# Optimization experiments

Measured on AMD Instinct MI355X. Metric: run time of the kernel, lower is better.

The kernel has to match this reference:

```python
import jax, jax.numpy as jnp
import numpy as np


def setup_inputs() -> dict:
    key = jax.random.key(0)
    ks = jax.random.split(key, 9)
    B, S, E, H, D = 8, 1000, 1024, 16, 64
    sc = 0.02
    return {
        "x": jax.random.normal(ks[0], (B, S, E), dtype=jnp.float32),
        "wq": jax.random.normal(ks[1], (H, E, D), dtype=jnp.float32) * sc,
        "bq": jax.random.normal(ks[2], (H, D), dtype=jnp.float32) * sc,
        "wk": jax.random.normal(ks[3], (H, E, D), dtype=jnp.float32) * sc,
        "bk": jax.random.normal(ks[4], (H, D), dtype=jnp.float32) * sc,
        "wv": jax.random.normal(ks[5], (H, E, D), dtype=jnp.float32) * sc,
        "bv": jax.random.normal(ks[6], (H, D), dtype=jnp.float32) * sc,
        "wp": jax.random.normal(ks[7], (E, E), dtype=jnp.float32) * sc,
        "bp": jax.random.normal(ks[8], (E,), dtype=jnp.float32) * sc,
    }


def reference(x, wq, bq, wk, bk, wv, bv, wp, bp):
    B, S, E = x.shape
    H, _, D = wq.shape
    # per-head projections, all heads batched: [B,H,S,D]
    q = jnp.einsum('bse,hed->bhsd', x, wq) + bq[None, :, None, :]
    k = jnp.einsum('bse,hed->bhsd', x, wk) + bk[None, :, None, :]
    v = jnp.einsum('bse,hed->bhsd', x, wv) + bv[None, :, None, :]
    # NOTE: original scales by sqrt(seq_len), not sqrt(head_dim)
    scores = jnp.einsum('bhsd,bhtd->bhst', q, k) / jnp.asarray(S, x.dtype) ** 0.5
    causal = jnp.tril(jnp.ones((S, S), dtype=bool))  # mask[:S,:S] == 1 keeps
    scores = jnp.where(causal, scores, jnp.asarray(-jnp.inf, x.dtype))
    attn = jax.nn.softmax(scores, axis=-1)
    z = jnp.einsum('bhst,bhtd->bhsd', attn, v)
    # concat heads in head order -> [B,S,E]
    y = z.transpose(0, 2, 1, 3).reshape(B, S, E)
    # projection then exact GELU (dropout is identity at eval)
    return jax.nn.gelu(jnp.einsum('bse,ef->bsf', y, wp) + bp, approximate=False)
```

## Files before the change

### kernel.cpp

```cpp
#include <hip/hip_runtime.h>
#include <hip/hip_bf16.h>
#include <math.h>

constexpr int B_ = 8, S_ = 1000, E_ = 1024, H_ = 16, D_ = 64;
constexpr int M_ = B_ * S_;

using bf16x8 = __attribute__((ext_vector_type(8))) __bf16;
using u16x8  = __attribute__((ext_vector_type(8))) unsigned short;
using f32x4  = __attribute__((ext_vector_type(4))) float;

static __device__ __forceinline__ unsigned short f2bf(float f) {
    union { float f; unsigned u; } c; c.f = f;
    return (unsigned short)((c.u + 0x7FFF + ((c.u >> 16) & 1)) >> 16);
}
static __device__ __forceinline__ unsigned short f2bf_fast(float f) {
    union { float f; unsigned u; } c; c.f = f;
    return (unsigned short)((c.u + 0x8000) >> 16);
}
static __device__ __forceinline__ float bfr2f(unsigned short s) {
    union { unsigned u; float f; } c; c.u = ((unsigned)s) << 16;
    return c.f;
}

__global__ __launch_bounds__(256) void cast_x_kernel(
    const float* __restrict__ x, unsigned short* __restrict__ xbf)
{
    const size_t i = ((size_t)blockIdx.x * 256 + threadIdx.x) * 4;
    float4 v = *(const float4*)(x + i);
    ushort4 o;
    o.x = f2bf(v.x); o.y = f2bf(v.y); o.z = f2bf(v.z); o.w = f2bf(v.w);
    *(ushort4*)(xbf + i) = o;
}

__global__ __launch_bounds__(256) void transpose_wqkv_kernel(
    const float* __restrict__ wq, const float* __restrict__ wk,
    const float* __restrict__ wv, unsigned short* __restrict__ WT)
{
    __shared__ unsigned short Ts[64 * 65];
    const int et = blockIdx.x, zh = blockIdx.y;
    const int z = zh >> 4, h = zh & 15;
    const float* src = (z == 0 ? wq : z == 1 ? wk : wv) + (size_t)h * E_ * D_;

    const int d = threadIdx.x & 63;
    const int e0 = threadIdx.x >> 6;
    #pragma unroll
    for (int p = 0; p < 16; ++p) {
        const int e = e0 + p * 4;
        Ts[d * 65 + e] = f2bf(src[(size_t)(et * 64 + e) * D_ + d]);
    }
    __syncthreads();
    const int e = threadIdx.x & 63;
    const int d0 = threadIdx.x >> 6;
    #pragma unroll
    for (int p = 0; p < 16; ++p) {
        const int dd = d0 + p * 4;
        WT[((size_t)zh * 64 + dd) * E_ + et * 64 + e] = Ts[dd * 65 + e];
    }
}

__global__ __launch_bounds__(256) void transpose_wp_kernel(
    const float* __restrict__ wp, unsigned short* __restrict__ wpT)
{
    __shared__ unsigned short Ts[64 * 65];
    const int et = blockIdx.x, ft = blockIdx.y;
    const int f = threadIdx.x & 63;
    const int e0 = threadIdx.x >> 6;
    #pragma unroll
    for (int p = 0; p < 16; ++p) {
        const int e = e0 + p * 4;
        Ts[f * 65 + e] = f2bf(wp[(size_t)(et * 64 + e) * E_ + ft * 64 + f]);
    }
    __syncthreads();
    const int e = threadIdx.x & 63;
    const int f0 = threadIdx.x >> 6;
    #pragma unroll
    for (int p = 0; p < 16; ++p) {
        const int ff = f0 + p * 4;
        wpT[((size_t)(ft * 64 + ff)) * E_ + et * 64 + e] = Ts[ff * 65 + e];
    }
}

__global__ __launch_bounds__(256) void transpose_v_kernel(
    const unsigned short* __restrict__ vb, unsigned short* __restrict__ vt)
{
    __shared__ unsigned short Ts[64 * 65];
    const int st = blockIdx.x, bh = blockIdx.y;
    const size_t ibase = (size_t)bh * S_ * D_;
    const size_t obase = (size_t)bh * D_ * S_;

    const int d = threadIdx.x & 63;
    const int s0 = threadIdx.x >> 6;
    #pragma unroll
    for (int p = 0; p < 16; ++p) {
        const int s = s0 + p * 4;
        const int srow = st * 64 + s;
        Ts[s * 65 + d] = (srow < S_) ? vb[ibase + (size_t)srow * D_ + d] : 0;
    }
    __syncthreads();
    const int s = threadIdx.x & 63;
    const int d0 = threadIdx.x >> 6;
    const int scol = st * 64 + s;
    if (scol < S_) {
        #pragma unroll
        for (int p = 0; p < 16; ++p) {
            const int dd = d0 + p * 4;
            vt[obase + (size_t)dd * S_ + scol] = Ts[s * 65 + dd];
        }
    }
}

__global__ __launch_bounds__(256) void qkv_mfma_kernel(
    const unsigned short* __restrict__ xbf, const unsigned short* __restrict__ WT,
    const float* __restrict__ bq, const float* __restrict__ bk,
    const float* __restrict__ bv,
    unsigned short* __restrict__ qb, unsigned short* __restrict__ kb,
    unsigned short* __restrict__ vb)
{
    constexpr int P = 72;
    __shared__ unsigned short As[128 * P];
    __shared__ unsigned short Bs[3][64 * P];

    const int tid = threadIdx.x;
    const int wave = tid >> 6, lane = tid & 63;
    const int m16 = lane & 15, quad = lane >> 4;
    const int m0 = blockIdx.x * 128;
    const int h  = blockIdx.y;

    f32x4 acc[3][4][2];
    #pragma unroll
    for (int z = 0; z < 3; ++z)
        #pragma unroll
        for (int nt = 0; nt < 4; ++nt)
            #pragma unroll
            for (int mh = 0; mh < 2; ++mh)
                acc[z][nt][mh] = (f32x4){0.f, 0.f, 0.f, 0.f};

    const int ar = tid & 31;
    const int ac8 = (tid >> 5) * 8;
    const int bd = tid & 63;
    const int bc8 = (tid >> 6) * 8;

    for (int kk = 0; kk < E_; kk += 64) {
        __syncthreads();
        #pragma unroll
        for (int p = 0; p < 4; ++p) {
            const int r = ar + p * 32;
            int srow = m0 + r; if (srow >= M_) srow = M_ - 1;
            *(u16x8*)&As[r * P + ac8] =
                *(const u16x8*)(xbf + (size_t)srow * E_ + kk + ac8);
        }
        #pragma unroll
        for (int z = 0; z < 3; ++z) {
            const unsigned short* wb = WT + ((size_t)(z * 16 + h) * 64 + bd) * E_ + kk;
            *(u16x8*)&Bs[z][bd * P + bc8]      = *(const u16x8*)(wb + bc8);
            *(u16x8*)&Bs[z][bd * P + bc8 + 32] = *(const u16x8*)(wb + bc8 + 32);
        }
        __syncthreads();

        #pragma unroll
        for (int kh = 0; kh < 2; ++kh) {
            const int ko = kh * 32 + quad * 8;
            const bf16x8 a0 = *(const bf16x8*)&As[(wave * 32 + m16) * P + ko];
            const bf16x8 a1 = *(const bf16x8*)&As[(wave * 32 + 16 + m16) * P + ko];
            #pragma unroll
            for (int z = 0; z < 3; ++z)
                #pragma unroll
                for (int nt = 0; nt < 4; ++nt) {
                    const bf16x8 bfr = *(const bf16x8*)&Bs[z][(nt * 16 + m16) * P + ko];
                    acc[z][nt][0] = __builtin_amdgcn_mfma_f32_16x16x32_bf16(a0, bfr, acc[z][nt][0], 0, 0, 0);
                    acc[z][nt][1] = __builtin_amdgcn_mfma_f32_16x16x32_bf16(a1, bfr, acc[z][nt][1], 0, 0, 0);
                }
        }
    }

    float biasv[3][4];
    #pragma unroll
    for (int nt = 0; nt < 4; ++nt) {
        biasv[0][nt] = bq[h * D_ + nt * 16 + m16];
        biasv[1][nt] = bk[h * D_ + nt * 16 + m16];
        biasv[2][nt] = bv[h * D_ + nt * 16 + m16];
    }

    #pragma unroll
    for (int mh = 0; mh < 2; ++mh)
        #pragma unroll
        for (int r = 0; r < 4; ++r) {
            const int row = m0 + wave * 32 + mh * 16 + quad * 4 + r;
            if (row < M_) {
                const int b = row / S_, s = row % S_;
                const size_t ob = (((size_t)b * H_ + h) * S_ + s) * D_ + m16;
                #pragma unroll
                for (int nt = 0; nt < 4; ++nt) {
                    qb[ob + nt * 16] = f2bf(acc[0][nt][mh][r] + biasv[0][nt]);
                    kb[ob + nt * 16] = f2bf(acc[1][nt][mh][r] + biasv[1][nt]);
                    vb[ob + nt * 16] = f2bf(acc[2][nt][mh][r] + biasv[2][nt]);
                }
            }
        }
}

__global__ __launch_bounds__(256) void attn_flash_kernel(
    const unsigned short* __restrict__ q, const unsigned short* __restrict__ k,
    const unsigned short* __restrict__ vt, unsigned short* __restrict__ ybf)
{
    constexpr int P_ = 72;
    __shared__ unsigned short Qs[64 * P_];
    __shared__ unsigned short Ks[64 * P_];
    __shared__ unsigned short Vt[64 * P_];
    __shared__ unsigned short Ps[4][16 * P_];

    const int tid  = threadIdx.x;
    const int wave = tid >> 6, lane = tid & 63;
    const int m16  = lane & 15, quad = lane >> 4;
    const int qt = (int)gridDim.x - 1 - (int)blockIdx.x;
    const int h = blockIdx.y, b = blockIdx.z;
    const size_t bh  = ((size_t)b * H_ + h) * S_;
    const size_t vtb = ((size_t)b * H_ + h) * (size_t)D_ * S_;
    const float sl2e = 0.031622776601683794f * 1.4426950408889634f;

    const int c8 = (tid & 7) * 8;
    const int r0 = tid >> 3;

    #pragma unroll
    for (int rr = 0; rr < 64; rr += 32) {
        const int r = r0 + rr;
        const int srow = qt * 64 + r;
        u16x8 val = {0, 0, 0, 0, 0, 0, 0, 0};
        if (srow < S_) val = *(const u16x8*)(q + (bh + srow) * D_ + c8);
        u16x8 o;
        #pragma unroll
        for (int j = 0; j < 8; ++j) o[j] = f2bf_fast(bfr2f(val[j]) * sl2e);
        *(u16x8*)&Qs[r * P_ + c8] = o;
    }
    __syncthreads();

    const bf16x8 qa0 = *(const bf16x8*)&Qs[(wave * 16 + m16) * P_ + quad * 8];
    const bf16x8 qa1 = *(const bf16x8*)&Qs[(wave * 16 + m16) * P_ + 32 + quad * 8];

    f32x4 O[4] = {{0,0,0,0},{0,0,0,0},{0,0,0,0},{0,0,0,0}};
    float l_i[4] = {0.f, 0.f, 0.f, 0.f};

    const int qrow_base = qt * 64 + wave * 16 + quad * 4;

    u16x8 kreg[2], vreg[2];
    #pragma unroll
    for (int i = 0; i < 2; ++i) {
        const int srow = r0 + i * 32;
        kreg[i] = *(const u16x8*)(k + (bh + srow) * D_ + c8);
        vreg[i] = *(const u16x8*)(vt + vtb + (size_t)(r0 + i * 32) * S_ + c8);
    }

    for (int tt = 0; tt <= qt; ++tt) {
        const int t0 = tt * 64;
        __syncthreads();
        #pragma unroll
        for (int i = 0; i < 2; ++i) {
            *(u16x8*)&Ks[(r0 + i * 32) * P_ + c8] = kreg[i];
            *(u16x8*)&Vt[(r0 + i * 32) * P_ + c8] = vreg[i];
        }
        __syncthreads();

        if (tt < qt) {
            const int nt0 = t0 + 64;
            #pragma unroll
            for (int i = 0; i < 2; ++i) {
                const int t = r0 + i * 32;
                const int srow = nt0 + t;
                u16x8 kv = {0,0,0,0,0,0,0,0}, vv = {0,0,0,0,0,0,0,0};
                if (srow < S_) kv = *(const u16x8*)(k + (bh + srow) * D_ + c8);
                if (nt0 + c8 < S_)
                    vv = *(const u16x8*)(vt + vtb + (size_t)t * S_ + nt0 + c8);
                kreg[i] = kv; vreg[i] = vv;
            }
        }

        f32x4 sc[4];
        #pragma unroll
        for (int ts = 0; ts < 4; ++ts) {
            const bf16x8 kb0 = *(const bf16x8*)&Ks[(ts * 16 + m16) * P_ + quad * 8];
            const bf16x8 kb1 = *(const bf16x8*)&Ks[(ts * 16 + m16) * P_ + 32 + quad * 8];
            f32x4 a = {0.f, 0.f, 0.f, 0.f};
            a = __builtin_amdgcn_mfma_f32_16x16x32_bf16(qa0, kb0, a, 0, 0, 0);
            a = __builtin_amdgcn_mfma_f32_16x16x32_bf16(qa1, kb1, a, 0, 0, 0);
            sc[ts] = a;
        }

        unsigned short* const pw = &Ps[wave][0];
        if (tt == qt) {
            #pragma unroll
            for (int ts = 0; ts < 4; ++ts) {
                const int t = t0 + ts * 16 + m16;
                #pragma unroll
                for (int r = 0; r < 4; ++r) {
                    float p = __builtin_amdgcn_exp2f(sc[ts][r]);
                    p = (t <= qrow_base + r) ? p : 0.f;
                    pw[(quad * 4 + r) * P_ + ts * 16 + m16] = f2bf_fast(p);
                    l_i[r] += p;
                }
            }
        } else {
            #pragma unroll
            for (int ts = 0; ts < 4; ++ts)
                #pragma unroll
                for (int r = 0; r < 4; ++r) {
                    const float p = __builtin_amdgcn_exp2f(sc[ts][r]);
                    pw[(quad * 4 + r) * P_ + ts * 16 + m16] = f2bf_fast(p);
                    l_i[r] += p;
                }
        }

        const bf16x8 pa0 = *(const bf16x8*)&pw[m16 * P_ + quad * 8];
        const bf16x8 pa1 = *(const bf16x8*)&pw[m16 * P_ + 32 + quad * 8];
        #pragma unroll
        for (int db = 0; db < 4; ++db) {
            const bf16x8 vb0 = *(const bf16x8*)&Vt[(db * 16 + m16) * P_ + quad * 8];
            const bf16x8 vb1 = *(const bf16x8*)&Vt[(db * 16 + m16) * P_ + 32 + quad * 8];
            O[db] = __builtin_amdgcn_mfma_f32_16x16x32_bf16(pa0, vb0, O[db], 0, 0, 0);
            O[db] = __builtin_amdgcn_mfma_f32_16x16x32_bf16(pa1, vb1, O[db], 0, 0, 0);
        }
    }

    #pragma unroll
    for (int off = 1; off < 16; off <<= 1)
        #pragma unroll
        for (int r = 0; r < 4; ++r)
            l_i[r] += __shfl_xor(l_i[r], off, 64);

    #pragma unroll
    for (int r = 0; r < 4; ++r) {
        const int qrow = qrow_base + r;
        if (qrow < S_) {
            const float invl = 1.0f / l_i[r];
            #pragma unroll
            for (int db = 0; db < 4; ++db)
                ybf[((size_t)b * S_ + qrow) * E_ + h * D_ + db * 16 + m16] =
                    f2bf(O[db][r] * invl);
        }
    }
}

__global__ __launch_bounds__(256) void proj_mfma_kernel(
    const unsigned short* __restrict__ ybf, const unsigned short* __restrict__ wpT,
    const float* __restrict__ bp, float* __restrict__ out)
{
    constexpr int P = 72;
    __shared__ unsigned short As[128 * P];
    __shared__ unsigned short Bs[128 * P];

    const int tid = threadIdx.x;
    const int wave = tid >> 6, lane = tid & 63;
    const int m16 = lane & 15, quad = lane >> 4;
    const int wm = wave >> 1, wn = wave & 1;
    const int m0 = blockIdx.x * 128;
    const int n0 = blockIdx.y * 128;

    f32x4 acc[4][4];
    #pragma unroll
    for (int nf = 0; nf < 4; ++nf)
        #pragma unroll
        for (int mf = 0; mf < 4; ++mf)
            acc[nf][mf] = (f32x4){0.f, 0.f, 0.f, 0.f};

    const int ar = tid & 31;
    const int ac8 = (tid >> 5) * 8;

    int asrow[4];
    #pragma unroll
    for (int p = 0; p < 4; ++p) {
        int r = m0 + ar + p * 32;
        asrow[p] = (r < M_) ? r : (M_ - 1);
    }

    u16x8 areg[4], breg[4];
    #pragma unroll
    for (int p = 0; p < 4; ++p) {
        areg[p] = *(const u16x8*)(ybf + (size_t)asrow[p] * E_ + ac8);
        breg[p] = *(const u16x8*)(wpT + (size_t)(n0 + ar + p * 32) * E_ + ac8);
    }

    for (int kk = 0; kk < E_; kk += 64) {
        __syncthreads();
        #pragma unroll
        for (int p = 0; p < 4; ++p) {
            *(u16x8*)&As[(ar + p * 32) * P + ac8] = areg[p];
            *(u16x8*)&Bs[(ar + p * 32) * P + ac8] = breg[p];
        }
        __syncthreads();

        if (kk + 64 < E_) {
            const int kn = kk + 64;
            #pragma unroll
            for (int p = 0; p < 4; ++p) {
                areg[p] = *(const u16x8*)(ybf + (size_t)asrow[p] * E_ + kn + ac8);
                breg[p] = *(const u16x8*)(wpT + (size_t)(n0 + ar + p * 32) * E_ + kn + ac8);
            }
        }

        #pragma unroll
        for (int kh = 0; kh < 2; ++kh) {
            const int ko = kh * 32 + quad * 8;
            bf16x8 af[4];
            #pragma unroll
            for (int mf = 0; mf < 4; ++mf)
                af[mf] = *(const bf16x8*)&As[(wm * 64 + mf * 16 + m16) * P + ko];
            #pragma unroll
            for (int nf = 0; nf < 4; ++nf) {
                const bf16x8 bfr = *(const bf16x8*)&Bs[(wn * 64 + nf * 16 + m16) * P + ko];
                #pragma unroll
                for (int mf = 0; mf < 4; ++mf)
                    acc[nf][mf] = __builtin_amdgcn_mfma_f32_16x16x32_bf16(
                        af[mf], bfr, acc[nf][mf], 0, 0, 0);
            }
        }
    }

    float biasv[4];
    #pragma unroll
    for (int nf = 0; nf < 4; ++nf)
        biasv[nf] = bp[n0 + wn * 64 + nf * 16 + m16];

    #pragma unroll
    for (int mf = 0; mf < 4; ++mf)
        #pragma unroll
        for (int r = 0; r < 4; ++r) {
            const int row = m0 + wm * 64 + mf * 16 + quad * 4 + r;
            if (row < M_) {
                #pragma unroll
                for (int nf = 0; nf < 4; ++nf) {
                    const int col = n0 + wn * 64 + nf * 16 + m16;
                    const float t = acc[nf][mf][r] + biasv[nf];
                    const float g = 0.5f * t * (1.0f + erff(t * 0.70710678118654752f));
                    out[(size_t)row * E_ + col] = g;
                }
            }
        }
}

extern "C" void kernel_launch(void* const* d_in, const int* in_sizes, int n_in,
                              void* d_out, int out_size, void* d_ws, size_t ws_size,
                              hipStream_t stream)
{
    const float* x  = (const float*)d_in[0];
    const float* wq = (const float*)d_in[1];
    const float* bq = (const float*)d_in[2];
    const float* wk = (const float*)d_in[3];
    const float* bk = (const float*)d_in[4];
    const float* wv = (const float*)d_in[5];
    const float* bv = (const float*)d_in[6];
    const float* wp = (const float*)d_in[7];
    const float* bp = (const float*)d_in[8];
    float* out = (float*)d_out;

    const size_t nME = (size_t)M_ * E_;
    unsigned short* xbf = (unsigned short*)d_ws;
    unsigned short* WT  = xbf + nME;
    unsigned short* wpT = WT + 3145728;
    unsigned short* qb  = wpT + 1048576;
    unsigned short* kb  = qb + nME;
    unsigned short* vb  = kb + nME;
    unsigned short* ybf = vb + nME;
    unsigned short* vtr = ybf + nME;

    cast_x_kernel<<<dim3((unsigned)(nME / 1024)), 256, 0, stream>>>(x, xbf);
    transpose_wqkv_kernel<<<dim3(16, 48), 256, 0, stream>>>(wq, wk, wv, WT);
    transpose_wp_kernel<<<dim3(16, 16), 256, 0, stream>>>(wp, wpT);

    qkv_mfma_kernel<<<dim3((M_ + 127) / 128, H_), 256, 0, stream>>>(
        xbf, WT, bq, bk, bv, qb, kb, vb);
    transpose_v_kernel<<<dim3(16, B_ * H_), 256, 0, stream>>>(vb, vtr);
    attn_flash_kernel<<<dim3((S_ + 63) / 64, H_, B_), 256, 0, stream>>>(
        qb, kb, vtr, ybf);
    proj_mfma_kernel<<<dim3((M_ + 127) / 128, E_ / 128), 256, 0, stream>>>(
        ybf, wpT, bp, out);
}
```

Measured before the change: 308.4 us.

## Retile QKV GEMM to square 128x128 tiles with direct global-to-LDS loads

The QKV projection kernel now treats the three weight sets as one 3072-wide N dimension and tiles it in 128x128 blocks with a 2x2 wave layout, instead of 128 rows x 3 heads' 64 columns per block. Tile loads use global_load_lds (direct global-to-LDS DMA) into unpadded LDS, which skips the register round trip. The grid's x axis now walks N tiles so neighbouring blocks share the same rows of x. The risk is LDS bank conflicts from dropping the padding, and a different accumulator register footprint.

```diff
diff --git a/kernel.cpp b/kernel.cpp
--- a/kernel.cpp
+++ b/kernel.cpp
@@ -20,6 +20,12 @@
 static __device__ __forceinline__ float bfr2f(unsigned short s) {
     union { unsigned u; float f; } c; c.u = ((unsigned)s) << 16;
     return c.f;
+}
+
+static __device__ __forceinline__ void gld16(const unsigned short* g, unsigned short* lds) {
+    __builtin_amdgcn_global_load_lds(
+        (__attribute__((address_space(1))) void*)(g),
+        (__attribute__((address_space(3))) void*)(lds), 16, 0, 0);
 }
 
 __global__ __launch_bounds__(256) void cast_x_kernel(
@@ -116,85 +122,82 @@
     unsigned short* __restrict__ qb, unsigned short* __restrict__ kb,
     unsigned short* __restrict__ vb)
 {
-    constexpr int P = 72;
-    __shared__ unsigned short As[128 * P];
-    __shared__ unsigned short Bs[3][64 * P];
-
-    const int tid = threadIdx.x;
+    __shared__ unsigned short As[128 * 64];
+    __shared__ unsigned short Bs[128 * 64];
+
+    const int tid  = threadIdx.x;
     const int wave = tid >> 6, lane = tid & 63;
-    const int m16 = lane & 15, quad = lane >> 4;
-    const int m0 = blockIdx.x * 128;
-    const int h  = blockIdx.y;
-
-    f32x4 acc[3][4][2];
-    #pragma unroll
-    for (int z = 0; z < 3; ++z)
-        #pragma unroll
-        for (int nt = 0; nt < 4; ++nt)
-            #pragma unroll
-            for (int mh = 0; mh < 2; ++mh)
-                acc[z][nt][mh] = (f32x4){0.f, 0.f, 0.f, 0.f};
-
-    const int ar = tid & 31;
-    const int ac8 = (tid >> 5) * 8;
-    const int bd = tid & 63;
-    const int bc8 = (tid >> 6) * 8;
+    const int m16  = lane & 15, quad = lane >> 4;
+    const int wm   = wave >> 1, wn = wave & 1;
+    const int n0   = blockIdx.x * 128;
+    const int m0   = blockIdx.y * 128;
+
+    f32x4 acc[4][4];
+    #pragma unroll
+    for (int nf = 0; nf < 4; ++nf)
+        #pragma unroll
+        for (int mf = 0; mf < 4; ++mf)
+            acc[nf][mf] = (f32x4){0.f, 0.f, 0.f, 0.f};
+
+    const int lrow = lane >> 3;
+    const int lcol = (lane & 7) << 3;
+
+    int a_srow[4];
+    #pragma unroll
+    for (int j = 0; j < 4; ++j) {
+        int r = m0 + (wave * 4 + j) * 8 + lrow;
+        a_srow[j] = (r < M_) ? r : (M_ - 1);
+    }
 
     for (int kk = 0; kk < E_; kk += 64) {
         __syncthreads();
         #pragma unroll
-        for (int p = 0; p < 4; ++p) {
-            const int r = ar + p * 32;
-            int srow = m0 + r; if (srow >= M_) srow = M_ - 1;
-            *(u16x8*)&As[r * P + ac8] =
-                *(const u16x8*)(xbf + (size_t)srow * E_ + kk + ac8);
-        }
-        #pragma unroll
-        for (int z = 0; z < 3; ++z) {
-            const unsigned short* wb = WT + ((size_t)(z * 16 + h) * 64 + bd) * E_ + kk;
-            *(u16x8*)&Bs[z][bd * P + bc8]      = *(const u16x8*)(wb + bc8);
-            *(u16x8*)&Bs[z][bd * P + bc8 + 32] = *(const u16x8*)(wb + bc8 + 32);
+        for (int j = 0; j < 4; ++j) {
+            const int i = wave * 4 + j;
+            gld16(xbf + (size_t)a_srow[j] * E_ + kk + lcol, &As[i * 512]);
+            gld16(WT + (size_t)(n0 + i * 8 + lrow) * E_ + kk + lcol, &Bs[i * 512]);
         }
         __syncthreads();
 
         #pragma unroll
         for (int kh = 0; kh < 2; ++kh) {
             const int ko = kh * 32 + quad * 8;
-            const bf16x8 a0 = *(const bf16x8*)&As[(wave * 32 + m16) * P + ko];
-            const bf16x8 a1 = *(const bf16x8*)&As[(wave * 32 + 16 + m16) * P + ko];
-            #pragma unroll
-            for (int z = 0; z < 3; ++z)
-                #pragma unroll
-                for (int nt = 0; nt < 4; ++nt) {
-                    const bf16x8 bfr = *(const bf16x8*)&Bs[z][(nt * 16 + m16) * P + ko];
-                    acc[z][nt][0] = __builtin_amdgcn_mfma_f32_16x16x32_bf16(a0, bfr, acc[z][nt][0], 0, 0, 0);
-                    acc[z][nt][1] = __builtin_amdgcn_mfma_f32_16x16x32_bf16(a1, bfr, acc[z][nt][1], 0, 0, 0);
-                }
-        }
-    }
-
-    float biasv[3][4];
-    #pragma unroll
-    for (int nt = 0; nt < 4; ++nt) {
-        biasv[0][nt] = bq[h * D_ + nt * 16 + m16];
-        biasv[1][nt] = bk[h * D_ + nt * 16 + m16];
-        biasv[2][nt] = bv[h * D_ + nt * 16 + m16];
-    }
-
-    #pragma unroll
-    for (int mh = 0; mh < 2; ++mh)
+            bf16x8 af[4];
+            #pragma unroll
+            for (int mf = 0; mf < 4; ++mf)
+                af[mf] = *(const bf16x8*)&As[(wm * 64 + mf * 16 + m16) * 64 + ko];
+            #pragma unroll
+            for (int nf = 0; nf < 4; ++nf) {
+                const bf16x8 bfr = *(const bf16x8*)&Bs[(wn * 64 + nf * 16 + m16) * 64 + ko];
+                #pragma unroll
+                for (int mf = 0; mf < 4; ++mf)
+                    acc[nf][mf] = __builtin_amdgcn_mfma_f32_16x16x32_bf16(
+                        af[mf], bfr, acc[nf][mf], 0, 0, 0);
+            }
+        }
+    }
+
+    const int z = n0 >> 10;
+    const int h = ((n0 >> 6) + wn) & 15;
+    unsigned short* const ob = (z == 0) ? qb : (z == 1) ? kb : vb;
+    const float* const bz    = (z == 0) ? bq : (z == 1) ? bk : bv;
+
+    float biasv[4];
+    #pragma unroll
+    for (int nf = 0; nf < 4; ++nf)
+        biasv[nf] = bz[h * D_ + nf * 16 + m16];
+
+    #pragma unroll
+    for (int mf = 0; mf < 4; ++mf)
         #pragma unroll
         for (int r = 0; r < 4; ++r) {
-            const int row = m0 + wave * 32 + mh * 16 + quad * 4 + r;
+            const int row = m0 + wm * 64 + mf * 16 + quad * 4 + r;
             if (row < M_) {
                 const int b = row / S_, s = row % S_;
-                const size_t ob = (((size_t)b * H_ + h) * S_ + s) * D_ + m16;
-                #pragma unroll
-                for (int nt = 0; nt < 4; ++nt) {
-                    qb[ob + nt * 16] = f2bf(acc[0][nt][mh][r] + biasv[0][nt]);
-                    kb[ob + nt * 16] = f2bf(acc[1][nt][mh][r] + biasv[1][nt]);
-                    vb[ob + nt * 16] = f2bf(acc[2][nt][mh][r] + biasv[2][nt]);
-                }
+                const size_t obase = (((size_t)b * H_ + h) * S_ + s) * D_ + m16;
+                #pragma unroll
+                for (int nf = 0; nf < 4; ++nf)
+                    ob[obase + nf * 16] = f2bf(acc[nf][mf][r] + biasv[nf]);
             }
         }
 }
@@ -465,7 +468,7 @@
     transpose_wqkv_kernel<<<dim3(16, 48), 256, 0, stream>>>(wq, wk, wv, WT);
     transpose_wp_kernel<<<dim3(16, 16), 256, 0, stream>>>(wp, wpT);
 
-    qkv_mfma_kernel<<<dim3((M_ + 127) / 128, H_), 256, 0, stream>>>(
+    qkv_mfma_kernel<<<dim3(3072 / 128, (M_ + 127) / 128), 256, 0, stream>>>(
         xbf, WT, bq, bk, bv, qb, kb, vb);
     transpose_v_kernel<<<dim3(16, B_ * H_), 256, 0, stream>>>(vb, vtr);
     attn_flash_kernel<<<dim3((S_ + 63) / 64, H_, B_), 256, 0, stream>>>(
```

After: 302.5 us. No clear change (-1.9%).
